# Kernel tuning notes

Measured on AMD Instinct MI355X. Metric: run time of the kernel, lower is better.

## Reference

```python
import jax, jax.numpy as jnp
import numpy as np

H = 128  # hidden_dim


def _lstm_layer(z, W_ih, W_hh, b_ih, b_hh):
    # z: [N, L, D] ; W_ih: [4H, D] ; W_hh: [4H, H] ; gate order i,f,g,o (PyTorch)
    N, L, _ = z.shape
    h_dim = W_hh.shape[1]
    # input contribution for all timesteps at once: [N, L, 4H]
    gx = jnp.einsum('nld,gd->nlg', z, W_ih) + b_ih + b_hh
    gx_t = jnp.swapaxes(gx, 0, 1)  # [L, N, 4H]

    def step(carry, g_t):
        h, c = carry
        g = g_t + h @ W_hh.T  # [N, 4H]
        i, f, gg, o = jnp.split(g, 4, axis=-1)
        i = jax.nn.sigmoid(i)
        f = jax.nn.sigmoid(f)
        gg = jnp.tanh(gg)
        o = jax.nn.sigmoid(o)
        c = f * c + i * gg
        h = o * jnp.tanh(c)
        return (h, c), h

    h0 = jnp.zeros((N, h_dim), z.dtype)
    (_, _), hs = jax.lax.scan(step, (h0, h0), gx_t)
    return jnp.swapaxes(hs, 0, 1)  # [N, L, H]


def setup_inputs() -> dict:
    key = jax.random.key(0)
    ks = jax.random.split(key, 16)
    N, L, D = 128, 2048, 64
    s = 1.0 / np.sqrt(H)  # PyTorch LSTM init scale
    u = lambda k, shp: jax.random.uniform(k, shp, jnp.float32, -s, s)
    inp = {
        'x': jax.random.normal(ks[0], (N, L, D), jnp.float32),
        'w': jax.random.uniform(ks[1], (N, L, D), jnp.float32),
        'W_ih1': u(ks[2], (4 * H, 2 * D)),
        'W_hh1': u(ks[3], (4 * H, H)),
        'b_ih1': u(ks[4], (4 * H,)),
        'b_hh1': u(ks[5], (4 * H,)),
        'W_ih2': u(ks[6], (4 * H, H)),
        'W_hh2': u(ks[7], (4 * H, H)),
        'b_ih2': u(ks[8], (4 * H,)),
        'b_hh2': u(ks[9], (4 * H,)),
        'W_ih3': u(ks[10], (4 * H, H)),
        'W_hh3': u(ks[11], (4 * H, H)),
        'b_ih3': u(ks[12], (4 * H,)),
        'b_hh3': u(ks[13], (4 * H,)),
        'W_lin': u(ks[14], (1, H)),
        'b_lin': u(ks[15], (1,)),
    }
    return inp


def reference(x, w, W_ih1, W_hh1, b_ih1, b_hh1, W_ih2, W_hh2, b_ih2, b_hh2,
              W_ih3, W_hh3, b_ih3, b_hh3, W_lin, b_lin):
    # concat x with w along feature dim -> [N, L, 2*in_dim]
    z = jnp.concatenate([x, w], axis=2).astype(jnp.float32)
    z = _lstm_layer(z, W_ih1, W_hh1, b_ih1, b_hh1)
    z = _lstm_layer(z, W_ih2, W_hh2, b_ih2, b_hh2)
    z = _lstm_layer(z, W_ih3, W_hh3, b_ih3, b_hh3)
    z = z @ W_lin.T + b_lin  # [N, L, out_dim]
    return z[:, -1]  # return_mode='last' -> [N, out_dim]
```

## Files before the change

### kernel.cpp

```cpp
#include <hip/hip_runtime.h>
#include <math.h>

#define N_BATCH 128
#define L_SEQ   2048
#define HD      128
#define G4      512

typedef __bf16 bf16x8 __attribute__((ext_vector_type(8)));
typedef float  f32x4  __attribute__((ext_vector_type(4)));

__device__ __forceinline__ float sigmoidf_fast(float x) {
    return __builtin_amdgcn_rcpf(1.0f + __expf(-x));
}
__device__ __forceinline__ float tanhf_fast(float x) {
    float a = fabsf(x);
    float t = 1.0f - 2.0f * __builtin_amdgcn_rcpf(1.0f + __expf(2.0f * a));
    return copysignf(t, x);
}
__device__ __forceinline__ void split8(const float* p, bf16x8& h, bf16x8& l) {
    #pragma unroll
    for (int e = 0; e < 8; ++e) {
        float v = p[e];
        __bf16 hb = (__bf16)v;
        h[e] = hb;
        l[e] = (__bf16)(v - (float)hb);
    }
}

__global__ void prep_split(const float* __restrict__ wh0, const float* __restrict__ wh1,
                           const float* __restrict__ wh2,
                           const float* __restrict__ wi0, const float* __restrict__ wi1,
                           const float* __restrict__ wi2,
                           const float* __restrict__ bi0, const float* __restrict__ bi1,
                           const float* __restrict__ bi2,
                           const float* __restrict__ bh0, const float* __restrict__ bh1,
                           const float* __restrict__ bh2,
                           __bf16* __restrict__ whh_hi, __bf16* __restrict__ whh_lo,
                           __bf16* __restrict__ wih_hi, __bf16* __restrict__ wih_lo,
                           float* __restrict__ bsum)
{
    int i = blockIdx.x * 256 + threadIdx.x;
    if (i < 196608) {
        int l = i >> 16;
        const float* src = (l == 0) ? wh0 : (l == 1) ? wh1 : wh2;
        float v = src[i & 65535];
        __bf16 h = (__bf16)v;
        whh_hi[i] = h; whh_lo[i] = (__bf16)(v - (float)h);
    } else {
        int j = i - 196608;
        int l = j >> 16;
        const float* src = (l == 0) ? wi0 : (l == 1) ? wi1 : wi2;
        float v = src[j & 65535];
        __bf16 h = (__bf16)v;
        wih_hi[j] = h; wih_lo[j] = (__bf16)(v - (float)h);
    }
    if (i < 1536) {
        int l = i >> 9, k = i & 511;
        const float* bi = (l == 0) ? bi0 : (l == 1) ? bi1 : bi2;
        const float* bh = (l == 0) ? bh0 : (l == 1) ? bh1 : bh2;
        bsum[i] = bi[k] + bh[k];
    }
}

__global__ __launch_bounds__(512, 2) void stage_kernel(
        const float* __restrict__ x, const float* __restrict__ w,
        const __bf16* __restrict__ whh_hi, const __bf16* __restrict__ whh_lo,
        const __bf16* __restrict__ wih_hi, const __bf16* __restrict__ wih_lo,
        const float* __restrict__ bsum,
        float* __restrict__ gxbase,
        __bf16* __restrict__ z1hi, __bf16* __restrict__ z1lo,
        __bf16* __restrict__ z2hi, __bf16* __restrict__ z2lo,
        float* __restrict__ carry,
        int d, int ct, int nchunk)
{
    const int bx = blockIdx.x;
    const int tid = threadIdx.x;
    const int wv = tid >> 6, lane = tid & 63, q = lane >> 4, cc = lane & 15;
    const size_t gxl = (size_t)ct * 65536;
    const size_t zchunk = (size_t)ct * 16384;

    __shared__ __align__(16) __bf16 hfhi[2][16][16][8];
    __shared__ __align__(16) __bf16 hflo[2][16][16][8];

    if (bx < 24) {
        const int lr = bx >> 3;
        const int cr = d - 2 * lr;
        if (cr < 0 || cr >= nchunk) return;
        const int sblk = bx & 7, sbase = sblk * 16;
        const int first = (cr == 0);
        const float* __restrict__ gx =
            gxbase + (size_t)((d & 1) * 3 + lr) * gxl + (size_t)sblk * 8192;
        __bf16* zho = (lr == 0) ? z1hi + (d & 1) * zchunk
                     : (lr == 1) ? z2hi + (d & 1) * zchunk : nullptr;
        __bf16* zlo_ = (lr == 0) ? z1lo + (d & 1) * zchunk
                      : (lr == 1) ? z2lo + (d & 1) * zchunk : nullptr;
        const __bf16* __restrict__ whi = whh_hi + (size_t)lr * 65536;
        const __bf16* __restrict__ wlo = whh_lo + (size_t)lr * 65536;
        float* __restrict__ hprev = carry + (size_t)lr * 16384;
        float* __restrict__ cst   = carry + (size_t)(3 + lr) * 16384;

        bf16x8 bh[4][4], bl[4][4];
        #pragma unroll
        for (int ti = 0; ti < 4; ++ti) {
            int ng = (wv + 8 * ti) * 16 + cc;
            #pragma unroll
            for (int ks = 0; ks < 4; ++ks) {
                bh[ti][ks] = *(const bf16x8*)(whi + (size_t)ng * HD + ks * 32 + q * 8);
                bl[ti][ks] = *(const bf16x8*)(wlo + (size_t)ng * HD + ks * 32 + q * 8);
            }
        }

        for (int i = tid; i < 2048; i += 512) {
            int m = i >> 7, u = i & 127;
            float v = first ? 0.f : hprev[(size_t)(sbase + m) * HD + u];
            __bf16 hb = (__bf16)v;
            hfhi[0][u >> 3][m][u & 7] = hb;
            hflo[0][u >> 3][m][u & 7] = (__bf16)(v - (float)hb);
        }
        const int uu = wv * 16 + cc;
        f32x4 cstate; cstate[0] = cstate[1] = cstate[2] = cstate[3] = 0.f;
        if (!first) {
            #pragma unroll
            for (int r = 0; r < 4; ++r)
                cstate[r] = cst[(size_t)(sbase + 4 * q + r) * HD + uu];
        }
        __syncthreads();

        f32x4 gcur[4];
        #pragma unroll
        for (int ti = 0; ti < 4; ++ti)
            gcur[ti] = *(const f32x4*)(gx + (size_t)((wv + 8 * ti) * 16 + cc) * 16 + 4 * q);

        float hv[4] = {0.f, 0.f, 0.f, 0.f};

        for (int tc = 0; tc < ct; ++tc) {
            const int rb = tc & 1, wb = rb ^ 1;
            const size_t off = (size_t)((tc + 1 < ct) ? tc + 1 : tc) * 65536;
            f32x4 gnx[4];
            #pragma unroll
            for (int ti = 0; ti < 4; ++ti)
                gnx[ti] = *(const f32x4*)(gx + off + (size_t)((wv + 8 * ti) * 16 + cc) * 16 + 4 * q);

            bf16x8 ahi[4], alo[4];
            #pragma unroll
            for (int ks = 0; ks < 4; ++ks) {
                ahi[ks] = *(const bf16x8*)&hfhi[rb][ks * 4 + q][cc][0];
                alo[ks] = *(const bf16x8*)&hflo[rb][ks * 4 + q][cc][0];
            }

            f32x4 acc[4];
            #pragma unroll
            for (int ti = 0; ti < 4; ++ti) {
                f32x4 dd = gcur[ti];
                #pragma unroll
                for (int ks = 0; ks < 4; ++ks)
                    dd = __builtin_amdgcn_mfma_f32_16x16x32_bf16(ahi[ks], bh[ti][ks], dd, 0, 0, 0);
                #pragma unroll
                for (int ks = 0; ks < 4; ++ks)
                    dd = __builtin_amdgcn_mfma_f32_16x16x32_bf16(ahi[ks], bl[ti][ks], dd, 0, 0, 0);
                #pragma unroll
                for (int ks = 0; ks < 4; ++ks)
                    dd = __builtin_amdgcn_mfma_f32_16x16x32_bf16(alo[ks], bh[ti][ks], dd, 0, 0, 0);
                acc[ti] = dd;
            }
            #pragma unroll
            for (int ti = 0; ti < 4; ++ti) gcur[ti] = gnx[ti];

            #pragma unroll
            for (int r = 0; r < 4; ++r) {
                float gi = sigmoidf_fast(acc[0][r]);
                float gf = sigmoidf_fast(acc[1][r]);
                float gg = tanhf_fast(acc[2][r]);
                float go = sigmoidf_fast(acc[3][r]);
                float cn = gf * cstate[r] + gi * gg;
                cstate[r] = cn;
                hv[r] = go * tanhf_fast(cn);
                __bf16 hb = (__bf16)hv[r];
                __bf16 lb = (__bf16)(hv[r] - (float)hb);
                int s = 4 * q + r;
                hfhi[wb][uu >> 3][s][uu & 7] = hb;
                hflo[wb][uu >> 3][s][uu & 7] = lb;
                if (lr < 2) {
                    size_t zi = ((size_t)tc * N_BATCH + sbase + s) * HD + uu;
                    zho[zi] = hb; zlo_[zi] = lb;
                }
            }
            __syncthreads();
        }
        #pragma unroll
        for (int r = 0; r < 4; ++r) {
            cst[(size_t)(sbase + 4 * q + r) * HD + uu] = cstate[r];
            hprev[(size_t)(sbase + 4 * q + r) * HD + uu] = hv[r];
        }
    } else {
        const int g = bx - 24;
        const int perl = 2 * ct;
        const int lg = g / perl;
        const int r0 = g - lg * perl;
        const int cg = d + 1 - 2 * lg;
        if (cg < 0 || cg >= nchunk) return;
        const int tg4 = r0 >> 3;
        const int gb = (r0 >> 1) & 3;
        const int nb = r0 & 1;

        const __bf16* zh = nullptr; const __bf16* zl = nullptr;
        if (lg > 0) {
            size_t po = (size_t)((d & 1) ^ 1) * zchunk;
            zh = ((lg == 1) ? z1hi : z2hi) + po;
            zl = ((lg == 1) ? z1lo : z2lo) + po;
        }

        const int mt0 = gb * 8 + (wv & 3) * 2;
        const int nt0 = (wv >> 2) * 2;

        bf16x8 ah[2][4], al[2][4];
        #pragma unroll
        for (int mm = 0; mm < 2; ++mm) {
            int row = (mt0 + mm) * 16 + cc;
            #pragma unroll
            for (int ks = 0; ks < 4; ++ks) {
                ah[mm][ks] = *(const bf16x8*)(wih_hi + (size_t)lg * 65536 + (size_t)row * HD + ks * 32 + q * 8);
                al[mm][ks] = *(const bf16x8*)(wih_lo + (size_t)lg * 65536 + (size_t)row * HD + ks * 32 + q * 8);
            }
        }

        float* __restrict__ gxo0 = gxbase + (size_t)(((d + 1) & 1) * 3 + lg) * gxl;

        for (int t4 = 0; t4 < 4; ++t4) {
            const int tc = tg4 * 4 + t4;
            bf16x8 zbh[2][4], zbl[2][4];
            #pragma unroll
            for (int nn = 0; nn < 2; ++nn) {
                int n = nb * 64 + (nt0 + nn) * 16 + cc;
                if (lg == 0) {
                    int tg = cg * ct + tc;
                    #pragma unroll
                    for (int ks = 0; ks < 4; ++ks) {
                        const float* src = (ks < 2 ? x : w)
                            + ((size_t)n * L_SEQ + tg) * 64 + (ks & 1) * 32 + q * 8;
                        split8(src, zbh[nn][ks], zbl[nn][ks]);
                    }
                } else {
                    size_t row = (size_t)tc * N_BATCH + n;
                    #pragma unroll
                    for (int ks = 0; ks < 4; ++ks) {
                        zbh[nn][ks] = *(const bf16x8*)(zh + row * HD + ks * 32 + q * 8);
                        zbl[nn][ks] = *(const bf16x8*)(zl + row * HD + ks * 32 + q * 8);
                    }
                }
            }

            f32x4 acc[2][2];
            #pragma unroll
            for (int mm = 0; mm < 2; ++mm)
                #pragma unroll
                for (int nn = 0; nn < 2; ++nn) {
                    f32x4 dd; dd[0] = dd[1] = dd[2] = dd[3] = 0.f;
                    #pragma unroll
                    for (int ks = 0; ks < 4; ++ks)
                        dd = __builtin_amdgcn_mfma_f32_16x16x32_bf16(ah[mm][ks], zbh[nn][ks], dd, 0, 0, 0);
                    #pragma unroll
                    for (int ks = 0; ks < 4; ++ks)
                        dd = __builtin_amdgcn_mfma_f32_16x16x32_bf16(ah[mm][ks], zbl[nn][ks], dd, 0, 0, 0);
                    #pragma unroll
                    for (int ks = 0; ks < 4; ++ks)
                        dd = __builtin_amdgcn_mfma_f32_16x16x32_bf16(al[mm][ks], zbh[nn][ks], dd, 0, 0, 0);
                    acc[mm][nn] = dd;
                }

            float* __restrict__ gxo = gxo0 + (size_t)tc * 65536;
            #pragma unroll
            for (int mm = 0; mm < 2; ++mm) {
                f32x4 bb = *(const f32x4*)(bsum + (size_t)lg * G4 + (mt0 + mm) * 16 + 4 * q);
                #pragma unroll
                for (int nn = 0; nn < 2; ++nn) {
                    int sb = nb * 4 + nt0 + nn;
                    #pragma unroll
                    for (int rr = 0; rr < 4; ++rr) {
                        int grow = (mt0 + mm) * 16 + 4 * q + rr;
                        gxo[(size_t)sb * 8192 + (size_t)grow * 16 + cc] = acc[mm][nn][rr] + bb[rr];
                    }
                }
            }
        }
    }
}

__global__ void final_lin(const float* __restrict__ hlast,
                          const float* __restrict__ Wlin,
                          const float* __restrict__ blin,
                          float* __restrict__ out)
{
    int n = threadIdx.x;
    const float4* h4 = (const float4*)(hlast + (size_t)n * HD);
    const float4* w4 = (const float4*)Wlin;
    float s = 0.f;
    #pragma unroll
    for (int k4 = 0; k4 < 32; ++k4) {
        float4 h = h4[k4];
        float4 ww = w4[k4];
        s += h.x * ww.x + h.y * ww.y + h.z * ww.z + h.w * ww.w;
    }
    out[n] = s + blin[0];
}

extern "C" void kernel_launch(void* const* d_in, const int* in_sizes, int n_in,
                              void* d_out, int out_size, void* d_ws, size_t ws_size,
                              hipStream_t stream)
{
    const float* x = (const float*)d_in[0];
    const float* w = (const float*)d_in[1];
    const float* Wih[3] = {(const float*)d_in[2], (const float*)d_in[6], (const float*)d_in[10]};
    const float* Whh[3] = {(const float*)d_in[3], (const float*)d_in[7], (const float*)d_in[11]};
    const float* bih[3] = {(const float*)d_in[4], (const float*)d_in[8], (const float*)d_in[12]};
    const float* bhh[3] = {(const float*)d_in[5], (const float*)d_in[9], (const float*)d_in[13]};
    const float* Wlin = (const float*)d_in[14];
    const float* blin = (const float*)d_in[15];
    float* out = (float*)d_out;

    int ct = 8;
    const int cands[4] = {64, 32, 16, 8};
    for (int i = 0; i < 4; ++i) {
        size_t need = 1835008ull * cands[i] + 2100000ull;
        if (need <= ws_size) { ct = cands[i]; break; }
    }
    const int nchunk = L_SEQ / ct;

    float* gxbase = (float*)d_ws;
    float* carry  = gxbase + (size_t)6 * ct * 65536;
    float* bsum   = carry + 98304;
    __bf16* whh_hi = (__bf16*)(bsum + 1536);
    __bf16* whh_lo = whh_hi + 196608;
    __bf16* wih_hi = whh_lo + 196608;
    __bf16* wih_lo = wih_hi + 196608;
    __bf16* z1hi = wih_lo + 196608;
    __bf16* z1lo = z1hi + (size_t)2 * ct * 16384;
    __bf16* z2hi = z1lo + (size_t)2 * ct * 16384;
    __bf16* z2lo = z2hi + (size_t)2 * ct * 16384;

    prep_split<<<dim3(1536), dim3(256), 0, stream>>>(
        Whh[0], Whh[1], Whh[2], Wih[0], Wih[1], Wih[2],
        bih[0], bih[1], bih[2], bhh[0], bhh[1], bhh[2],
        whh_hi, whh_lo, wih_hi, wih_lo, bsum);

    const int nblk = 24 + 6 * ct;
    for (int d = -1; d <= nchunk + 3; ++d) {
        stage_kernel<<<dim3(nblk), dim3(512), 0, stream>>>(
            x, w, whh_hi, whh_lo, wih_hi, wih_lo, bsum,
            gxbase, z1hi, z1lo, z2hi, z2lo, carry, d, ct, nchunk);
    }
    final_lin<<<dim3(1), dim3(128), 0, stream>>>(carry + 2 * 16384, Wlin, blin, out);
}
```

Measured before the change: 3.684 ms.

## Unroll recurrence by two, use lightweight LDS barrier, store z as fp32, allow larger chunks

The recurrent loop is unrolled by two with fixed LDS ping-pong buffers, two register sets of prefetched gate inputs, and gx loads issued after the MFMAs. __syncthreads is replaced by an inline s_waitcnt lgkmcnt(0)+s_barrier. Layer outputs are stored once as fp32 and split into hi/lo bf16 in the input-projection blocks, so the recurrent step writes one value instead of two. A ct=128 chunk size is allowed to cut kernel launches, at the cost of more workspace and an unroll that assumes ct is even.

```diff
diff --git a/kernel.cpp b/kernel.cpp
--- a/kernel.cpp
+++ b/kernel.cpp
@@ -25,6 +25,9 @@
         h[e] = hb;
         l[e] = (__bf16)(v - (float)hb);
     }
+}
+__device__ __forceinline__ void lds_barrier() {
+    asm volatile("s_waitcnt lgkmcnt(0)\n\ts_barrier" ::: "memory");
 }
 
 __global__ void prep_split(const float* __restrict__ wh0, const float* __restrict__ wh1,
@@ -68,8 +71,7 @@
         const __bf16* __restrict__ wih_hi, const __bf16* __restrict__ wih_lo,
         const float* __restrict__ bsum,
         float* __restrict__ gxbase,
-        __bf16* __restrict__ z1hi, __bf16* __restrict__ z1lo,
-        __bf16* __restrict__ z2hi, __bf16* __restrict__ z2lo,
+        float* __restrict__ z1, float* __restrict__ z2,
         float* __restrict__ carry,
         int d, int ct, int nchunk)
 {
@@ -90,10 +92,8 @@
         const int first = (cr == 0);
         const float* __restrict__ gx =
             gxbase + (size_t)((d & 1) * 3 + lr) * gxl + (size_t)sblk * 8192;
-        __bf16* zho = (lr == 0) ? z1hi + (d & 1) * zchunk
-                     : (lr == 1) ? z2hi + (d & 1) * zchunk : nullptr;
-        __bf16* zlo_ = (lr == 0) ? z1lo + (d & 1) * zchunk
-                      : (lr == 1) ? z2lo + (d & 1) * zchunk : nullptr;
+        float* zo = (lr == 0) ? z1 + (d & 1) * zchunk
+                   : (lr == 1) ? z2 + (d & 1) * zchunk : nullptr;
         const __bf16* __restrict__ whi = whh_hi + (size_t)lr * 65536;
         const __bf16* __restrict__ wlo = whh_lo + (size_t)lr * 65536;
         float* __restrict__ hprev = carry + (size_t)lr * 16384;
@@ -126,66 +126,118 @@
         }
         __syncthreads();
 
-        f32x4 gcur[4];
+        const size_t go[4] = {
+            (size_t)((wv + 0) * 16 + cc) * 16 + 4 * q,
+            (size_t)((wv + 8) * 16 + cc) * 16 + 4 * q,
+            (size_t)((wv + 16) * 16 + cc) * 16 + 4 * q,
+            (size_t)((wv + 24) * 16 + cc) * 16 + 4 * q };
+
+        f32x4 ga[4], gb_[4];
         #pragma unroll
-        for (int ti = 0; ti < 4; ++ti)
-            gcur[ti] = *(const f32x4*)(gx + (size_t)((wv + 8 * ti) * 16 + cc) * 16 + 4 * q);
+        for (int ti = 0; ti < 4; ++ti) ga[ti] = *(const f32x4*)(gx + go[ti]);
+        {
+            int t1 = (1 < ct) ? 1 : 0;
+            #pragma unroll
+            for (int ti = 0; ti < 4; ++ti)
+                gb_[ti] = *(const f32x4*)(gx + (size_t)t1 * 65536 + go[ti]);
+        }
 
         float hv[4] = {0.f, 0.f, 0.f, 0.f};
 
-        for (int tc = 0; tc < ct; ++tc) {
-            const int rb = tc & 1, wb = rb ^ 1;
-            const size_t off = (size_t)((tc + 1 < ct) ? tc + 1 : tc) * 65536;
-            f32x4 gnx[4];
-            #pragma unroll
-            for (int ti = 0; ti < 4; ++ti)
-                gnx[ti] = *(const f32x4*)(gx + off + (size_t)((wv + 8 * ti) * 16 + cc) * 16 + 4 * q);
-
-            bf16x8 ahi[4], alo[4];
-            #pragma unroll
-            for (int ks = 0; ks < 4; ++ks) {
-                ahi[ks] = *(const bf16x8*)&hfhi[rb][ks * 4 + q][cc][0];
-                alo[ks] = *(const bf16x8*)&hflo[rb][ks * 4 + q][cc][0];
-            }
-
-            f32x4 acc[4];
-            #pragma unroll
-            for (int ti = 0; ti < 4; ++ti) {
-                f32x4 dd = gcur[ti];
-                #pragma unroll
-                for (int ks = 0; ks < 4; ++ks)
-                    dd = __builtin_amdgcn_mfma_f32_16x16x32_bf16(ahi[ks], bh[ti][ks], dd, 0, 0, 0);
-                #pragma unroll
-                for (int ks = 0; ks < 4; ++ks)
-                    dd = __builtin_amdgcn_mfma_f32_16x16x32_bf16(ahi[ks], bl[ti][ks], dd, 0, 0, 0);
-                #pragma unroll
-                for (int ks = 0; ks < 4; ++ks)
-                    dd = __builtin_amdgcn_mfma_f32_16x16x32_bf16(alo[ks], bh[ti][ks], dd, 0, 0, 0);
-                acc[ti] = dd;
-            }
-            #pragma unroll
-            for (int ti = 0; ti < 4; ++ti) gcur[ti] = gnx[ti];
-
-            #pragma unroll
-            for (int r = 0; r < 4; ++r) {
-                float gi = sigmoidf_fast(acc[0][r]);
-                float gf = sigmoidf_fast(acc[1][r]);
-                float gg = tanhf_fast(acc[2][r]);
-                float go = sigmoidf_fast(acc[3][r]);
-                float cn = gf * cstate[r] + gi * gg;
-                cstate[r] = cn;
-                hv[r] = go * tanhf_fast(cn);
-                __bf16 hb = (__bf16)hv[r];
-                __bf16 lb = (__bf16)(hv[r] - (float)hb);
-                int s = 4 * q + r;
-                hfhi[wb][uu >> 3][s][uu & 7] = hb;
-                hflo[wb][uu >> 3][s][uu & 7] = lb;
-                if (lr < 2) {
-                    size_t zi = ((size_t)tc * N_BATCH + sbase + s) * HD + uu;
-                    zho[zi] = hb; zlo_[zi] = lb;
-                }
-            }
-            __syncthreads();
+        for (int tc = 0; tc < ct; tc += 2) {
+            {
+                bf16x8 ahi[4], alo[4];
+                #pragma unroll
+                for (int ks = 0; ks < 4; ++ks) {
+                    ahi[ks] = *(const bf16x8*)&hfhi[0][ks * 4 + q][cc][0];
+                    alo[ks] = *(const bf16x8*)&hflo[0][ks * 4 + q][cc][0];
+                }
+                f32x4 acc[4];
+                #pragma unroll
+                for (int ti = 0; ti < 4; ++ti) {
+                    f32x4 dd = ga[ti];
+                    #pragma unroll
+                    for (int ks = 0; ks < 4; ++ks)
+                        dd = __builtin_amdgcn_mfma_f32_16x16x32_bf16(ahi[ks], bh[ti][ks], dd, 0, 0, 0);
+                    #pragma unroll
+                    for (int ks = 0; ks < 4; ++ks)
+                        dd = __builtin_amdgcn_mfma_f32_16x16x32_bf16(ahi[ks], bl[ti][ks], dd, 0, 0, 0);
+                    #pragma unroll
+                    for (int ks = 0; ks < 4; ++ks)
+                        dd = __builtin_amdgcn_mfma_f32_16x16x32_bf16(alo[ks], bh[ti][ks], dd, 0, 0, 0);
+                    acc[ti] = dd;
+                }
+                {
+                    int tn = (tc + 2 < ct) ? tc + 2 : tc;
+                    #pragma unroll
+                    for (int ti = 0; ti < 4; ++ti)
+                        ga[ti] = *(const f32x4*)(gx + (size_t)tn * 65536 + go[ti]);
+                }
+                #pragma unroll
+                for (int r = 0; r < 4; ++r) {
+                    float gi = sigmoidf_fast(acc[0][r]);
+                    float gf = sigmoidf_fast(acc[1][r]);
+                    float gg = tanhf_fast(acc[2][r]);
+                    float go_ = sigmoidf_fast(acc[3][r]);
+                    float cn = gf * cstate[r] + gi * gg;
+                    cstate[r] = cn;
+                    hv[r] = go_ * tanhf_fast(cn);
+                    __bf16 hb = (__bf16)hv[r];
+                    int s = 4 * q + r;
+                    hfhi[1][uu >> 3][s][uu & 7] = hb;
+                    hflo[1][uu >> 3][s][uu & 7] = (__bf16)(hv[r] - (float)hb);
+                    if (lr < 2)
+                        zo[((size_t)tc * N_BATCH + sbase + s) * HD + uu] = hv[r];
+                }
+                lds_barrier();
+            }
+            {
+                const int t1 = tc + 1;
+                bf16x8 ahi[4], alo[4];
+                #pragma unroll
+                for (int ks = 0; ks < 4; ++ks) {
+                    ahi[ks] = *(const bf16x8*)&hfhi[1][ks * 4 + q][cc][0];
+                    alo[ks] = *(const bf16x8*)&hflo[1][ks * 4 + q][cc][0];
+                }
+                f32x4 acc[4];
+                #pragma unroll
+                for (int ti = 0; ti < 4; ++ti) {
+                    f32x4 dd = gb_[ti];
+                    #pragma unroll
+                    for (int ks = 0; ks < 4; ++ks)
+                        dd = __builtin_amdgcn_mfma_f32_16x16x32_bf16(ahi[ks], bh[ti][ks], dd, 0, 0, 0);
+                    #pragma unroll
+                    for (int ks = 0; ks < 4; ++ks)
+                        dd = __builtin_amdgcn_mfma_f32_16x16x32_bf16(ahi[ks], bl[ti][ks], dd, 0, 0, 0);
+                    #pragma unroll
+                    for (int ks = 0; ks < 4; ++ks)
+                        dd = __builtin_amdgcn_mfma_f32_16x16x32_bf16(alo[ks], bh[ti][ks], dd, 0, 0, 0);
+                    acc[ti] = dd;
+                }
+                {
+                    int tn = (tc + 3 < ct) ? tc + 3 : tc;
+                    #pragma unroll
+                    for (int ti = 0; ti < 4; ++ti)
+                        gb_[ti] = *(const f32x4*)(gx + (size_t)tn * 65536 + go[ti]);
+                }
+                #pragma unroll
+                for (int r = 0; r < 4; ++r) {
+                    float gi = sigmoidf_fast(acc[0][r]);
+                    float gf = sigmoidf_fast(acc[1][r]);
+                    float gg = tanhf_fast(acc[2][r]);
+                    float go_ = sigmoidf_fast(acc[3][r]);
+                    float cn = gf * cstate[r] + gi * gg;
+                    cstate[r] = cn;
+                    hv[r] = go_ * tanhf_fast(cn);
+                    __bf16 hb = (__bf16)hv[r];
+                    int s = 4 * q + r;
+                    hfhi[0][uu >> 3][s][uu & 7] = hb;
+                    hflo[0][uu >> 3][s][uu & 7] = (__bf16)(hv[r] - (float)hb);
+                    if (lr < 2)
+                        zo[((size_t)t1 * N_BATCH + sbase + s) * HD + uu] = hv[r];
+                }
+                lds_barrier();
+            }
         }
         #pragma unroll
         for (int r = 0; r < 4; ++r) {
@@ -203,11 +255,10 @@
         const int gb = (r0 >> 1) & 3;
         const int nb = r0 & 1;
 
-        const __bf16* zh = nullptr; const __bf16* zl = nullptr;
+        const float* zsrc = nullptr;
         if (lg > 0) {
             size_t po = (size_t)((d & 1) ^ 1) * zchunk;
-            zh = ((lg == 1) ? z1hi : z2hi) + po;
-            zl = ((lg == 1) ? z1lo : z2lo) + po;
+            zsrc = ((lg == 1) ? z1 : z2) + po;
         }
 
         const int mt0 = gb * 8 + (wv & 3) * 2;
@@ -241,12 +292,10 @@
                         split8(src, zbh[nn][ks], zbl[nn][ks]);
                     }
                 } else {
-                    size_t row = (size_t)tc * N_BATCH + n;
-                    #pragma unroll
-                    for (int ks = 0; ks < 4; ++ks) {
-                        zbh[nn][ks] = *(const bf16x8*)(zh + row * HD + ks * 32 + q * 8);
-                        zbl[nn][ks] = *(const bf16x8*)(zl + row * HD + ks * 32 + q * 8);
-                    }
+                    const float* src0 = zsrc + ((size_t)tc * N_BATCH + n) * HD;
+                    #pragma unroll
+                    for (int ks = 0; ks < 4; ++ks)
+                        split8(src0 + ks * 32 + q * 8, zbh[nn][ks], zbl[nn][ks]);
                 }
             }
 
@@ -319,9 +368,9 @@
     float* out = (float*)d_out;
 
     int ct = 8;
-    const int cands[4] = {64, 32, 16, 8};
-    for (int i = 0; i < 4; ++i) {
-        size_t need = 1835008ull * cands[i] + 2100000ull;
+    const int cands[5] = {128, 64, 32, 16, 8};
+    for (int i = 0; i < 5; ++i) {
+        size_t need = 1835008ull * cands[i] + 2200000ull;
         if (need <= ws_size) { ct = cands[i]; break; }
     }
     const int nchunk = L_SEQ / ct;
@@ -333,10 +382,8 @@
     __bf16* whh_lo = whh_hi + 196608;
     __bf16* wih_hi = whh_lo + 196608;
     __bf16* wih_lo = wih_hi + 196608;
-    __bf16* z1hi = wih_lo + 196608;
-    __bf16* z1lo = z1hi + (size_t)2 * ct * 16384;
-    __bf16* z2hi = z1lo + (size_t)2 * ct * 16384;
-    __bf16* z2lo = z2hi + (size_t)2 * ct * 16384;
+    float* z1 = (float*)(wih_lo + 196608);
+    float* z2 = z1 + (size_t)2 * ct * 16384;
 
     prep_split<<<dim3(1536), dim3(256), 0, stream>>>(
         Whh[0], Whh[1], Whh[2], Wih[0], Wih[1], Wih[2],
@@ -347,7 +394,7 @@
     for (int d = -1; d <= nchunk + 3; ++d) {
         stage_kernel<<<dim3(nblk), dim3(512), 0, stream>>>(
             x, w, whh_hi, whh_lo, wih_hi, wih_lo, bsum,
-            gxbase, z1hi, z1lo, z2hi, z2lo, carry, d, ct, nchunk);
+            gxbase, z1, z2, carry, d, ct, nchunk);
     }
     final_lin<<<dim3(1), dim3(128), 0, stream>>>(carry + 2 * 16384, Wlin, blin, out);
 }
```

After: 3.810 ms. 3.4% more time.
